# Kernel tuning notes

Measured on AMD Instinct MI355X. Metric: run time of the kernel, lower is better.

## Reference

```python
import jax, jax.numpy as jnp
import numpy as np

TEMPERATURE = 8.0  # sqrt(d_k), d_k = 64


def setup_inputs() -> dict:
    key = jax.random.key(0)
    kq, kk, kv = jax.random.split(key, 3)
    BH, N, D = 16, 4096, 64  # batch*heads, seq_len, head_dim
    q = jax.random.normal(kq, (BH, N, D), dtype=jnp.float32)
    k = jax.random.normal(kk, (BH, N, D), dtype=jnp.float32)
    v = jax.random.normal(kv, (BH, N, D), dtype=jnp.float32)
    # causal mask: True means masked (filled with -inf), broadcast over BH
    mask = jnp.triu(jnp.ones((N, N), dtype=jnp.bool_), k=1)[None, :, :]
    return {"q": q, "k": k, "v": v, "mask": mask}


def reference(q, k, v, mask):
    # attn = q @ k^T / temperature, masked softmax, attn @ v
    scores = jnp.einsum("bnd,bmd->bnm", q, k) / TEMPERATURE
    scores = jnp.where(mask, -jnp.inf, scores)
    attn = jax.nn.softmax(scores, axis=-1)  # dropout p=0 (eval) -> identity
    out = jnp.einsum("bnm,bmd->bnd", attn, v)
    return out, attn
```

## Files before the change

### kernel.cpp

```cpp
#include <hip/hip_runtime.h>

typedef float f32x4 __attribute__((ext_vector_type(4)));
typedef __bf16 bf16x8 __attribute__((ext_vector_type(8)));
typedef unsigned short u16x8 __attribute__((ext_vector_type(8)));
typedef unsigned int u32x4 __attribute__((ext_vector_type(4)));

#define NBH 16
#define NSEQ 4096
#define DH 64

__device__ __forceinline__ unsigned int cvtpk(float lo, float hi) {
  unsigned int r;
  asm("v_cvt_pk_bf16_f32 %0, %1, %2" : "=v"(r) : "v"(lo), "v"(hi));
  return r;
}
__device__ __forceinline__ bf16x8 pk8(const float* f) {
  union { unsigned int u[4]; bf16x8 b; } x;
#pragma unroll
  for (int i = 0; i < 4; ++i) x.u[i] = cvtpk(f[2 * i], f[2 * i + 1]);
  return x.b;
}

__device__ __forceinline__ void lbar() {
  __builtin_amdgcn_sched_barrier(0);
  asm volatile("s_waitcnt lgkmcnt(0)" ::: "memory");
  __builtin_amdgcn_s_barrier();
  __builtin_amdgcn_sched_barrier(0);
}

__global__ __launch_bounds__(512, 4) void sdpa_fused(
    const float* __restrict__ qg, const float* __restrict__ kg,
    const float* __restrict__ vg, float* __restrict__ outg) {
  const int bid = blockIdx.x;
  const int xcd = bid & 7;
  const int ii = bid >> 3;
  const int hh = ii >> 5;
  const int qt = ii & 31;
  const int b = 2 * xcd + hh;
  const int qa = qt, qb = 63 - qt;

  const int tid = threadIdx.x;
  const int w = tid >> 6, lane = tid & 63;
  const int g = lane >> 4, c = lane & 15;
  const int grp = w >> 2;
  const int wr0 = 16 * (w & 3);
  const int qrw = (grp ? qb : qa) * 64;
  const int kmax = grp ? qb : qa;
  const int pOff = 16 * w;

  const float* qbp = qg + (size_t)b * NSEQ * DH;
  const float* kbp = kg + (size_t)b * NSEQ * DH;
  const float* vbp = vg + (size_t)b * NSEQ * DH;
  float* outb = outg + (size_t)b * NSEQ * DH;
  float* attnb = outg + (size_t)NBH * NSEQ * DH + (size_t)b * NSEQ * NSEQ;

  __shared__ unsigned short Kl[2][64][72];
  __shared__ unsigned int Vt[2][64][37];
  __shared__ unsigned short Pl[128][72];

  bf16x8 aq[2];
  {
    const float* qrow = qbp + (size_t)(qrw + wr0 + c) * DH;
#pragma unroll
    for (int ks = 0; ks < 2; ++ks) {
      float f[8];
      *(float4*)f = *(const float4*)(qrow + 32 * ks + 8 * g);
      *(float4*)(f + 4) = *(const float4*)(qrow + 32 * ks + 8 * g + 4);
      aq[ks] = pk8(f);
    }
  }

  const int kj = tid >> 3, kcs = tid & 7;
  const int vp = tid >> 4, dch = tid & 15;
  float kf[8], vf0[4], vf1[4];

  auto loadK = [&](int kt) {
    const float* s = kbp + (size_t)(kt * 64 + kj) * DH + kcs * 8;
    *(float4*)kf = ((const float4*)s)[0];
    *(float4*)(kf + 4) = ((const float4*)s)[1];
  };
  auto writeK = [&](int cur) {
    u32x4 u;
#pragma unroll
    for (int i = 0; i < 4; ++i) u[i] = cvtpk(kf[2 * i], kf[2 * i + 1]);
    *(u32x4*)&Kl[cur][kj][kcs * 8] = u;
  };
  auto loadV = [&](int kt) {
    const float* s0 = vbp + (size_t)(kt * 64 + 2 * vp) * DH + dch * 4;
    *(float4*)vf0 = *(const float4*)s0;
    *(float4*)vf1 = *(const float4*)(s0 + DH);
  };
  auto writeV = [&](int cur) {
#pragma unroll
    for (int e = 0; e < 4; ++e) Vt[cur][4 * dch + e][vp] = cvtpk(vf0[e], vf1[e]);
  };

  float part[4] = {0.f, 0.f, 0.f, 0.f};
  loadK(0);
  for (int kt = 0; kt <= qb; ++kt) {
    const int cur = kt & 1;
    writeK(cur);
    lbar();
    if (kt < qb) loadK(kt + 1);
    if (kt <= kmax) {
      f32x4 acc[4];
#pragma unroll
      for (int ct = 0; ct < 4; ++ct) acc[ct] = (f32x4){0.f, 0.f, 0.f, 0.f};
#pragma unroll
      for (int ks = 0; ks < 2; ++ks)
#pragma unroll
        for (int ct = 0; ct < 4; ++ct) {
          u16x8 u = *(const u16x8*)&Kl[cur][16 * ct + c][32 * ks + 8 * g];
          acc[ct] = __builtin_amdgcn_mfma_f32_16x16x32_bf16(aq[ks], __builtin_bit_cast(bf16x8, u), acc[ct], 0, 0, 0);
        }
#pragma unroll
      for (int ct = 0; ct < 4; ++ct)
#pragma unroll
        for (int r = 0; r < 4; ++r) {
          const int j = kt * 64 + 16 * ct + c;
          const int i = qrw + wr0 + 4 * g + r;
          part[r] += (j <= i) ? __expf(acc[ct][r] * 0.125f) : 0.f;
        }
    }
  }
  float rinv[4];
#pragma unroll
  for (int r = 0; r < 4; ++r) {
    float s = part[r];
    s += __shfl_xor(s, 1); s += __shfl_xor(s, 2);
    s += __shfl_xor(s, 4); s += __shfl_xor(s, 8);
    rinv[r] = 1.f / s;
  }

  __syncthreads();

  loadK(0);
  loadV(0);
  f32x4 oacc[4];
#pragma unroll
  for (int ct = 0; ct < 4; ++ct) oacc[ct] = (f32x4){0.f, 0.f, 0.f, 0.f};

  for (int kt = 0; kt <= qb; ++kt) {
    const int cur = kt & 1;
    writeK(cur);
    writeV(cur);
    lbar();
    if (kt < qb) { loadK(kt + 1); loadV(kt + 1); }

    if (kt <= kmax) {
      f32x4 acc[4];
#pragma unroll
      for (int ct = 0; ct < 4; ++ct) acc[ct] = (f32x4){0.f, 0.f, 0.f, 0.f};
#pragma unroll
      for (int ks = 0; ks < 2; ++ks)
#pragma unroll
        for (int ct = 0; ct < 4; ++ct) {
          u16x8 u = *(const u16x8*)&Kl[cur][16 * ct + c][32 * ks + 8 * g];
          acc[ct] = __builtin_amdgcn_mfma_f32_16x16x32_bf16(aq[ks], __builtin_bit_cast(bf16x8, u), acc[ct], 0, 0, 0);
        }

#pragma unroll
      for (int ct = 0; ct < 4; ++ct)
#pragma unroll
        for (int r = 0; r < 4; ++r) {
          const int jl = 16 * ct + c;
          const int i = qrw + wr0 + 4 * g + r;
          const int j = kt * 64 + jl;
          const float p = (j <= i) ? __expf(acc[ct][r] * 0.125f) * rinv[r] : 0.f;
          Pl[pOff + 4 * g + r][jl] = (unsigned short)cvtpk(p, p);
          attnb[(size_t)i * NSEQ + j] = p;
        }

      bf16x8 ap[2];
#pragma unroll
      for (int ks = 0; ks < 2; ++ks)
        ap[ks] = __builtin_bit_cast(bf16x8, *(const u16x8*)&Pl[pOff + c][32 * ks + 8 * g]);
#pragma unroll
      for (int ks = 0; ks < 2; ++ks)
#pragma unroll
        for (int ct = 0; ct < 4; ++ct) {
          u16x8 bv = *(const u16x8*)&Vt[cur][16 * ct + c][16 * ks + 4 * g];
          oacc[ct] = __builtin_amdgcn_mfma_f32_16x16x32_bf16(ap[ks], __builtin_bit_cast(bf16x8, bv), oacc[ct], 0, 0, 0);
        }
    }
  }

#pragma unroll
  for (int ct = 0; ct < 4; ++ct)
#pragma unroll
    for (int r = 0; r < 4; ++r) {
      const int i = qrw + wr0 + 4 * g + r;
      outb[(size_t)i * DH + 16 * ct + c] = oacc[ct][r];
    }

  const float4 z = {0.f, 0.f, 0.f, 0.f};
#pragma unroll
  for (int t = 0; t < 2; ++t) {
    const int q0 = t ? qb : qa;
    const int zc0 = 64 * (q0 + 1);
    if (zc0 < NSEQ) {
      const int zw4 = (NSEQ - zc0) >> 2;
      for (int r = 0; r < 64; ++r) {
        float4* dst = (float4*)(attnb + (size_t)(q0 * 64 + r) * NSEQ + zc0);
        for (int c4 = tid; c4 < zw4; c4 += 512) dst[c4] = z;
      }
    }
  }
}

extern "C" void kernel_launch(void* const* d_in, const int* in_sizes, int n_in,
                              void* d_out, int out_size, void* d_ws, size_t ws_size,
                              hipStream_t stream) {
  (void)in_sizes; (void)n_in; (void)out_size; (void)d_ws; (void)ws_size;
  const float* q = (const float*)d_in[0];
  const float* k = (const float*)d_in[1];
  const float* v = (const float*)d_in[2];
  float* out = (float*)d_out;
  sdpa_fused<<<dim3(512), dim3(512), 0, stream>>>(q, k, v, out);
}
```

Measured before the change: 324.4 us.

## Use 128-key tiles for row-sum pass and vectorized nontemporal attn stores

The first (row-sum) pass now stages 128 keys per iteration in a larger shared buffer that is unioned with the second-pass buffers, halving its barrier count. The attention matrix is now written from the bf16 P tile in shared memory as contiguous 16-float nontemporal vector stores per lane instead of scattered scalar stores. Output and zero-fill stores are also made nontemporal. The attn values written are now bf16-rounded, which lowers the output precision.

```diff
diff --git a/kernel.cpp b/kernel.cpp
--- a/kernel.cpp
+++ b/kernel.cpp
@@ -20,12 +20,17 @@
   for (int i = 0; i < 4; ++i) x.u[i] = cvtpk(f[2 * i], f[2 * i + 1]);
   return x.b;
 }
-
+__device__ __forceinline__ float bf2f(unsigned short h) {
+  return __uint_as_float(((unsigned int)h) << 16);
+}
 __device__ __forceinline__ void lbar() {
   __builtin_amdgcn_sched_barrier(0);
   asm volatile("s_waitcnt lgkmcnt(0)" ::: "memory");
   __builtin_amdgcn_s_barrier();
   __builtin_amdgcn_sched_barrier(0);
+}
+__device__ __forceinline__ void ntst4(float* p, f32x4 v) {
+  __builtin_nontemporal_store(v, (f32x4*)p);
 }
 
 __global__ __launch_bounds__(512, 4) void sdpa_fused(
@@ -46,6 +51,7 @@
   const int wr0 = 16 * (w & 3);
   const int qrw = (grp ? qb : qa) * 64;
   const int kmax = grp ? qb : qa;
+  const int kmax2 = kmax >> 1;
   const int pOff = 16 * w;
 
   const float* qbp = qg + (size_t)b * NSEQ * DH;
@@ -54,9 +60,14 @@
   float* outb = outg + (size_t)b * NSEQ * DH;
   float* attnb = outg + (size_t)NBH * NSEQ * DH + (size_t)b * NSEQ * NSEQ;
 
-  __shared__ unsigned short Kl[2][64][72];
-  __shared__ unsigned int Vt[2][64][37];
-  __shared__ unsigned short Pl[128][72];
+  __shared__ union {
+    unsigned short K2[2][128][72];
+    struct {
+      unsigned short Kl[2][64][72];
+      unsigned int Vt[2][64][37];
+      unsigned short Pl[128][72];
+    } m;
+  } sm;
 
   bf16x8 aq[2];
   {
@@ -70,130 +81,164 @@
     }
   }
 
-  const int kj = tid >> 3, kcs = tid & 7;
-  const int vp = tid >> 4, dch = tid & 15;
-  float kf[8], vf0[4], vf1[4];
-
-  auto loadK = [&](int kt) {
-    const float* s = kbp + (size_t)(kt * 64 + kj) * DH + kcs * 8;
-    *(float4*)kf = ((const float4*)s)[0];
-    *(float4*)(kf + 4) = ((const float4*)s)[1];
-  };
-  auto writeK = [&](int cur) {
-    u32x4 u;
-#pragma unroll
-    for (int i = 0; i < 4; ++i) u[i] = cvtpk(kf[2 * i], kf[2 * i + 1]);
-    *(u32x4*)&Kl[cur][kj][kcs * 8] = u;
-  };
-  auto loadV = [&](int kt) {
-    const float* s0 = vbp + (size_t)(kt * 64 + 2 * vp) * DH + dch * 4;
-    *(float4*)vf0 = *(const float4*)s0;
-    *(float4*)vf1 = *(const float4*)(s0 + DH);
-  };
-  auto writeV = [&](int cur) {
-#pragma unroll
-    for (int e = 0; e < 4; ++e) Vt[cur][4 * dch + e][vp] = cvtpk(vf0[e], vf1[e]);
-  };
-
-  float part[4] = {0.f, 0.f, 0.f, 0.f};
-  loadK(0);
-  for (int kt = 0; kt <= qb; ++kt) {
-    const int cur = kt & 1;
-    writeK(cur);
-    lbar();
-    if (kt < qb) loadK(kt + 1);
-    if (kt <= kmax) {
-      f32x4 acc[4];
-#pragma unroll
-      for (int ct = 0; ct < 4; ++ct) acc[ct] = (f32x4){0.f, 0.f, 0.f, 0.f};
-#pragma unroll
-      for (int ks = 0; ks < 2; ++ks)
-#pragma unroll
-        for (int ct = 0; ct < 4; ++ct) {
-          u16x8 u = *(const u16x8*)&Kl[cur][16 * ct + c][32 * ks + 8 * g];
-          acc[ct] = __builtin_amdgcn_mfma_f32_16x16x32_bf16(aq[ks], __builtin_bit_cast(bf16x8, u), acc[ct], 0, 0, 0);
+  float rinv[4];
+
+  {
+    const int r0 = tid >> 2, ch = tid & 3;
+    float kf2[16];
+    auto loadK2 = [&](int s2) {
+      const float* s = kbp + (size_t)(s2 * 128 + r0) * DH + ch * 16;
+#pragma unroll
+      for (int i = 0; i < 4; ++i) *(float4*)(kf2 + 4 * i) = ((const float4*)s)[i];
+    };
+    auto writeK2 = [&](int cur) {
+      unsigned int* dst = (unsigned int*)&sm.K2[cur][r0][ch * 16];
+#pragma unroll
+      for (int i = 0; i < 8; ++i) dst[i] = cvtpk(kf2[2 * i], kf2[2 * i + 1]);
+    };
+
+    const int nst1 = (qb >> 1) + 1;
+    float part[4] = {0.f, 0.f, 0.f, 0.f};
+    loadK2(0);
+    for (int s2 = 0; s2 < nst1; ++s2) {
+      const int cur = s2 & 1;
+      writeK2(cur);
+      lbar();
+      if (s2 + 1 < nst1) loadK2(s2 + 1);
+      if (s2 <= kmax2) {
+#pragma unroll
+        for (int cg = 0; cg < 2; ++cg) {
+          f32x4 acc[4];
+#pragma unroll
+          for (int cc = 0; cc < 4; ++cc) acc[cc] = (f32x4){0.f, 0.f, 0.f, 0.f};
+#pragma unroll
+          for (int ks = 0; ks < 2; ++ks)
+#pragma unroll
+            for (int cc = 0; cc < 4; ++cc) {
+              u16x8 u = *(const u16x8*)&sm.K2[cur][16 * (4 * cg + cc) + c][32 * ks + 8 * g];
+              acc[cc] = __builtin_amdgcn_mfma_f32_16x16x32_bf16(aq[ks], __builtin_bit_cast(bf16x8, u), acc[cc], 0, 0, 0);
+            }
+#pragma unroll
+          for (int cc = 0; cc < 4; ++cc)
+#pragma unroll
+            for (int r = 0; r < 4; ++r) {
+              const int j = s2 * 128 + 16 * (4 * cg + cc) + c;
+              const int i = qrw + wr0 + 4 * g + r;
+              part[r] += (j <= i) ? __expf(acc[cc][r] * 0.125f) : 0.f;
+            }
         }
-#pragma unroll
-      for (int ct = 0; ct < 4; ++ct)
-#pragma unroll
-        for (int r = 0; r < 4; ++r) {
-          const int j = kt * 64 + 16 * ct + c;
-          const int i = qrw + wr0 + 4 * g + r;
-          part[r] += (j <= i) ? __expf(acc[ct][r] * 0.125f) : 0.f;
+      }
+    }
+#pragma unroll
+    for (int r = 0; r < 4; ++r) {
+      float s = part[r];
+      s += __shfl_xor(s, 1); s += __shfl_xor(s, 2);
+      s += __shfl_xor(s, 4); s += __shfl_xor(s, 8);
+      rinv[r] = 1.f / s;
+    }
+  }
+
+  __syncthreads();
+
+  {
+    const int kj = tid >> 3, kcs = tid & 7;
+    const int vp = tid >> 4, dch = tid & 15;
+    float kf[8], vf0[4], vf1[4];
+
+    auto loadK = [&](int kt) {
+      const float* s = kbp + (size_t)(kt * 64 + kj) * DH + kcs * 8;
+      *(float4*)kf = ((const float4*)s)[0];
+      *(float4*)(kf + 4) = ((const float4*)s)[1];
+    };
+    auto writeK = [&](int cur) {
+      u32x4 u;
+#pragma unroll
+      for (int i = 0; i < 4; ++i) u[i] = cvtpk(kf[2 * i], kf[2 * i + 1]);
+      *(u32x4*)&sm.m.Kl[cur][kj][kcs * 8] = u;
+    };
+    auto loadV = [&](int kt) {
+      const float* s0 = vbp + (size_t)(kt * 64 + 2 * vp) * DH + dch * 4;
+      *(float4*)vf0 = *(const float4*)s0;
+      *(float4*)vf1 = *(const float4*)(s0 + DH);
+    };
+    auto writeV = [&](int cur) {
+#pragma unroll
+      for (int e = 0; e < 4; ++e) sm.m.Vt[cur][4 * dch + e][vp] = cvtpk(vf0[e], vf1[e]);
+    };
+
+    loadK(0);
+    loadV(0);
+    f32x4 oacc[4];
+#pragma unroll
+    for (int ct = 0; ct < 4; ++ct) oacc[ct] = (f32x4){0.f, 0.f, 0.f, 0.f};
+
+    for (int kt = 0; kt <= qb; ++kt) {
+      const int cur = kt & 1;
+      writeK(cur);
+      writeV(cur);
+      lbar();
+      if (kt < qb) { loadK(kt + 1); loadV(kt + 1); }
+
+      if (kt <= kmax) {
+        f32x4 acc[4];
+#pragma unroll
+        for (int ct = 0; ct < 4; ++ct) acc[ct] = (f32x4){0.f, 0.f, 0.f, 0.f};
+#pragma unroll
+        for (int ks = 0; ks < 2; ++ks)
+#pragma unroll
+          for (int ct = 0; ct < 4; ++ct) {
+            u16x8 u = *(const u16x8*)&sm.m.Kl[cur][16 * ct + c][32 * ks + 8 * g];
+            acc[ct] = __builtin_amdgcn_mfma_f32_16x16x32_bf16(aq[ks], __builtin_bit_cast(bf16x8, u), acc[ct], 0, 0, 0);
+          }
+
+#pragma unroll
+        for (int ct = 0; ct < 4; ++ct)
+#pragma unroll
+          for (int r = 0; r < 4; ++r) {
+            const int jl = 16 * ct + c;
+            const int i = qrw + wr0 + 4 * g + r;
+            const int j = kt * 64 + jl;
+            const float p = (j <= i) ? __expf(acc[ct][r] * 0.125f) * rinv[r] : 0.f;
+            sm.m.Pl[pOff + 4 * g + r][jl] = (unsigned short)cvtpk(p, p);
+          }
+
+        {
+          const int lr = lane >> 2, lc = lane & 3;
+          u16x8 u0 = *(const u16x8*)&sm.m.Pl[pOff + lr][lc * 16];
+          u16x8 u1 = *(const u16x8*)&sm.m.Pl[pOff + lr][lc * 16 + 8];
+          float* dst = attnb + (size_t)(qrw + wr0 + lr) * NSEQ + kt * 64 + lc * 16;
+          f32x4 f0, f1, f2, f3;
+          f0[0] = bf2f(u0[0]); f0[1] = bf2f(u0[1]); f0[2] = bf2f(u0[2]); f0[3] = bf2f(u0[3]);
+          f1[0] = bf2f(u0[4]); f1[1] = bf2f(u0[5]); f1[2] = bf2f(u0[6]); f1[3] = bf2f(u0[7]);
+          f2[0] = bf2f(u1[0]); f2[1] = bf2f(u1[1]); f2[2] = bf2f(u1[2]); f2[3] = bf2f(u1[3]);
+          f3[0] = bf2f(u1[4]); f3[1] = bf2f(u1[5]); f3[2] = bf2f(u1[6]); f3[3] = bf2f(u1[7]);
+          ntst4(dst, f0); ntst4(dst + 4, f1); ntst4(dst + 8, f2); ntst4(dst + 12, f3);
         }
-    }
-  }
-  float rinv[4];
-#pragma unroll
-  for (int r = 0; r < 4; ++r) {
-    float s = part[r];
-    s += __shfl_xor(s, 1); s += __shfl_xor(s, 2);
-    s += __shfl_xor(s, 4); s += __shfl_xor(s, 8);
-    rinv[r] = 1.f / s;
-  }
-
-  __syncthreads();
-
-  loadK(0);
-  loadV(0);
-  f32x4 oacc[4];
-#pragma unroll
-  for (int ct = 0; ct < 4; ++ct) oacc[ct] = (f32x4){0.f, 0.f, 0.f, 0.f};
-
-  for (int kt = 0; kt <= qb; ++kt) {
-    const int cur = kt & 1;
-    writeK(cur);
-    writeV(cur);
-    lbar();
-    if (kt < qb) { loadK(kt + 1); loadV(kt + 1); }
-
-    if (kt <= kmax) {
-      f32x4 acc[4];
-#pragma unroll
-      for (int ct = 0; ct < 4; ++ct) acc[ct] = (f32x4){0.f, 0.f, 0.f, 0.f};
-#pragma unroll
-      for (int ks = 0; ks < 2; ++ks)
-#pragma unroll
-        for (int ct = 0; ct < 4; ++ct) {
-          u16x8 u = *(const u16x8*)&Kl[cur][16 * ct + c][32 * ks + 8 * g];
-          acc[ct] = __builtin_amdgcn_mfma_f32_16x16x32_bf16(aq[ks], __builtin_bit_cast(bf16x8, u), acc[ct], 0, 0, 0);
-        }
-
-#pragma unroll
-      for (int ct = 0; ct < 4; ++ct)
-#pragma unroll
-        for (int r = 0; r < 4; ++r) {
-          const int jl = 16 * ct + c;
-          const int i = qrw + wr0 + 4 * g + r;
-          const int j = kt * 64 + jl;
-          const float p = (j <= i) ? __expf(acc[ct][r] * 0.125f) * rinv[r] : 0.f;
-          Pl[pOff + 4 * g + r][jl] = (unsigned short)cvtpk(p, p);
-          attnb[(size_t)i * NSEQ + j] = p;
-        }
-
-      bf16x8 ap[2];
-#pragma unroll
-      for (int ks = 0; ks < 2; ++ks)
-        ap[ks] = __builtin_bit_cast(bf16x8, *(const u16x8*)&Pl[pOff + c][32 * ks + 8 * g]);
-#pragma unroll
-      for (int ks = 0; ks < 2; ++ks)
-#pragma unroll
-        for (int ct = 0; ct < 4; ++ct) {
-          u16x8 bv = *(const u16x8*)&Vt[cur][16 * ct + c][16 * ks + 4 * g];
-          oacc[ct] = __builtin_amdgcn_mfma_f32_16x16x32_bf16(ap[ks], __builtin_bit_cast(bf16x8, bv), oacc[ct], 0, 0, 0);
-        }
-    }
-  }
-
-#pragma unroll
-  for (int ct = 0; ct < 4; ++ct)
-#pragma unroll
-    for (int r = 0; r < 4; ++r) {
-      const int i = qrw + wr0 + 4 * g + r;
-      outb[(size_t)i * DH + 16 * ct + c] = oacc[ct][r];
-    }
-
-  const float4 z = {0.f, 0.f, 0.f, 0.f};
+
+        bf16x8 ap[2];
+#pragma unroll
+        for (int ks = 0; ks < 2; ++ks)
+          ap[ks] = __builtin_bit_cast(bf16x8, *(const u16x8*)&sm.m.Pl[pOff + c][32 * ks + 8 * g]);
+#pragma unroll
+        for (int ks = 0; ks < 2; ++ks)
+#pragma unroll
+          for (int ct = 0; ct < 4; ++ct) {
+            u16x8 bv = *(const u16x8*)&sm.m.Vt[cur][16 * ct + c][16 * ks + 4 * g];
+            oacc[ct] = __builtin_amdgcn_mfma_f32_16x16x32_bf16(ap[ks], __builtin_bit_cast(bf16x8, bv), oacc[ct], 0, 0, 0);
+          }
+      }
+    }
+
+#pragma unroll
+    for (int ct = 0; ct < 4; ++ct)
+#pragma unroll
+      for (int r = 0; r < 4; ++r) {
+        const int i = qrw + wr0 + 4 * g + r;
+        __builtin_nontemporal_store(oacc[ct][r], &outb[(size_t)i * DH + 16 * ct + c]);
+      }
+  }
+
+  const f32x4 z = {0.f, 0.f, 0.f, 0.f};
 #pragma unroll
   for (int t = 0; t < 2; ++t) {
     const int q0 = t ? qb : qa;
@@ -201,8 +246,8 @@
     if (zc0 < NSEQ) {
       const int zw4 = (NSEQ - zc0) >> 2;
       for (int r = 0; r < 64; ++r) {
-        float4* dst = (float4*)(attnb + (size_t)(q0 * 64 + r) * NSEQ + zc0);
-        for (int c4 = tid; c4 < zw4; c4 += 512) dst[c4] = z;
+        float* dst = attnb + (size_t)(q0 * 64 + r) * NSEQ + zc0;
+        for (int c4 = tid; c4 < zw4; c4 += 512) ntst4(dst + 4 * c4, z);
       }
     }
   }
```

After: 765.4 us. 136% more time.
